# Optimization experiments

Hardware: AMD Instinct MI355X
Metric: run time of the kernel (lower is better)

The kernel has to match this reference:

```python
import jax, jax.numpy as jnp
import numpy as np

B, N1, N2, D, R = 4, 128, 128, 256, 4


def setup_inputs() -> dict:
    key = jax.random.key(0)
    ks = jax.random.split(key, 8)
    s = 0.02  # small init scale for weights
    return {
        "features1": jax.random.normal(ks[0], (B, N1, D), jnp.float32),
        "features2": jax.random.normal(ks[1], (B, N2, D), jnp.float32),
        # relation nets stacked over R: Linear(2D->D), Linear(D->D//2), Linear(D//2->1)
        "W1": jax.random.normal(ks[2], (R, 2 * D, D), jnp.float32) * s,
        "b1": jnp.zeros((R, D), jnp.float32),
        "W2": jax.random.normal(ks[3], (R, D, D // 2), jnp.float32) * s,
        "b2": jnp.zeros((R, D // 2), jnp.float32),
        "w3": jax.random.normal(ks[4], (R, D // 2), jnp.float32) * s,
        "b3": jnp.zeros((R,), jnp.float32),
        # aggregator: Linear(D*R -> 2D), Linear(2D -> D)
        "Wa1": jax.random.normal(ks[5], (D * R, 2 * D), jnp.float32) * s,
        "ba1": jnp.zeros((2 * D,), jnp.float32),
        "Wa2": jax.random.normal(ks[6], (2 * D, D), jnp.float32) * s,
        "ba2": jnp.zeros((D,), jnp.float32),
    }


def reference(features1, features2, W1, b1, W2, b2, w3, b3, Wa1, ba1, Wa2, ba2):
    b, n1, d = features1.shape
    n2 = features2.shape[1]
    r = W1.shape[0]
    # concat([f1_i, f2_j]) @ W1 == f1_i @ W1[:d] + f2_j @ W1[d:]
    W1a, W1b = W1[:, :d, :], W1[:, d:, :]
    h1 = jnp.einsum('bid,rde->brie', features1, W1a)          # [B,R,N1,D]
    h2 = jnp.einsum('bjd,rde->brje', features2, W1b)          # [B,R,N2,D]
    h = jax.nn.relu(h1[:, :, :, None, :] + h2[:, :, None, :, :]
                    + b1[None, :, None, None, :])             # [B,R,N1,N2,D]
    g = jax.nn.relu(jnp.einsum('brijd,rde->brije', h, W2)
                    + b2[None, :, None, None, :])             # [B,R,N1,N2,D//2]
    scores = jnp.einsum('brije,re->brij', g, w3) + b3[None, :, None, None]
    w = jax.nn.softmax(scores, axis=-1)                       # softmax over j (N2)
    rel = jnp.einsum('brij,bjd->brid', w, features2)          # [B,R,N1,D]
    # torch cat over relations along feature dim -> relation index outermost
    all_rel = rel.transpose(0, 2, 1, 3).reshape(b, n1, r * d)  # [B,N1,R*D]
    out = jax.nn.relu(all_rel @ Wa1 + ba1) @ Wa2 + ba2         # [B,N1,D]
    return out
```

## Files before the change

kernel.cpp:

```cpp
#include <hip/hip_runtime.h>


typedef _Float16 f16x8 __attribute__((ext_vector_type(8)));
typedef float f32x16 __attribute__((ext_vector_type(16)));

static __device__ __forceinline__ ushort f2h(float f) {
  _Float16 h = (_Float16)f;
  return __builtin_bit_cast(ushort, h);
}
static __device__ __forceinline__ uint pack2(float a, float b) {
  return (uint)f2h(a) | ((uint)f2h(b) << 16);
}
static __device__ __forceinline__ uint pk_add(uint a, uint b) {
  uint r;
  asm("v_pk_add_f16 %0, %1, %2" : "=v"(r) : "v"(a), "v"(b));
  return r;
}
static __device__ __forceinline__ uint pk_relu(uint a) {
  uint r;
  asm("v_pk_max_f16 %0, %1, %2" : "=v"(r) : "v"(a), "v"(0u));
  return r;
}

template<int KBLK>
static __device__ __forceinline__ void gemm32x64_body(
    const float* __restrict__ A, const float* __restrict__ W,
    float* __restrict__ Cout, int K, int N, int rt, int ct, int k0)
{
  int t = threadIdx.x;
  int tm2 = t >> 4;
  int tn4 = t & 15;
  int arow = t >> 3;
  int akq = (t & 7) * 4;
  int bk = t >> 4;
  int bn4 = (t & 15) * 4;
  __shared__ __align__(16) float As[32][33];
  __shared__ __align__(16) float Bs[32][64];

  const float* Ab = A + (size_t)(rt * 32 + arow) * K + k0;
  const float* Wb = W + (size_t)k0 * N + ct * 64 + bn4;

  float4 pa = *(const float4*)&Ab[akq];
  float4 pb0 = *(const float4*)&Wb[(size_t)bk * N];
  float4 pb1 = *(const float4*)&Wb[(size_t)(bk + 16) * N];

  float acc[2][4];
  #pragma unroll
  for (int i = 0; i < 2; ++i)
    #pragma unroll
    for (int j = 0; j < 4; ++j) acc[i][j] = 0.f;

  for (int kc = 0; kc < KBLK; kc += 32) {
    __syncthreads();
    As[akq + 0][arow] = pa.x;
    As[akq + 1][arow] = pa.y;
    As[akq + 2][arow] = pa.z;
    As[akq + 3][arow] = pa.w;
    *(float4*)&Bs[bk][bn4] = pb0;
    *(float4*)&Bs[bk + 16][bn4] = pb1;
    __syncthreads();
    if (kc + 32 < KBLK) {
      pa  = *(const float4*)&Ab[kc + 32 + akq];
      pb0 = *(const float4*)&Wb[(size_t)(kc + 32 + bk) * N];
      pb1 = *(const float4*)&Wb[(size_t)(kc + 32 + bk + 16) * N];
    }
    #pragma unroll
    for (int kk = 0; kk < 32; ++kk) {
      float2 a = *(const float2*)&As[kk][tm2 * 2];
      float4 w = *(const float4*)&Bs[kk][tn4 * 4];
      acc[0][0] = fmaf(a.x, w.x, acc[0][0]); acc[0][1] = fmaf(a.x, w.y, acc[0][1]);
      acc[0][2] = fmaf(a.x, w.z, acc[0][2]); acc[0][3] = fmaf(a.x, w.w, acc[0][3]);
      acc[1][0] = fmaf(a.y, w.x, acc[1][0]); acc[1][1] = fmaf(a.y, w.y, acc[1][1]);
      acc[1][2] = fmaf(a.y, w.z, acc[1][2]); acc[1][3] = fmaf(a.y, w.w, acc[1][3]);
    }
  }

  int col = ct * 64 + tn4 * 4;
  #pragma unroll
  for (int qm = 0; qm < 2; ++qm) {
    int row = rt * 32 + tm2 * 2 + qm;
    float4 ov = make_float4(acc[qm][0], acc[qm][1], acc[qm][2], acc[qm][3]);
    *(float4*)&Cout[(size_t)row * N + col] = ov;
  }
}

template<int KBLK>
__global__ __launch_bounds__(256) void gemm_part(
    const float* __restrict__ A, const float* __restrict__ W,
    float* __restrict__ part, int K, int N, int M)
{
  int kp = blockIdx.z;
  gemm32x64_body<KBLK>(A, W, part + (size_t)kp * M * N, K, N,
                       blockIdx.y, blockIdx.x, kp * KBLK);
}

__global__ __launch_bounds__(256) void gemm2_fused(
    const float* __restrict__ p1, const float* __restrict__ ba1,
    const float* __restrict__ W, float* __restrict__ part)
{
  const int K = 512, N = 256, KBLK = 128;
  int rt = blockIdx.y, ct = blockIdx.x, kp = blockIdx.z;
  int k0 = kp * KBLK;
  float* Cout = part + (size_t)kp * 512 * N;
  int t = threadIdx.x;
  int tm2 = t >> 4;
  int tn4 = t & 15;
  int arow = t >> 3;
  int akq = (t & 7) * 4;
  int bk = t >> 4;
  int bn4 = (t & 15) * 4;
  __shared__ __align__(16) float As[32][33];
  __shared__ __align__(16) float Bs[32][64];

  const float* Ap = p1 + (size_t)(rt * 32 + arow) * K;
  const float* Wb = W + (size_t)k0 * N + ct * 64 + bn4;

  auto loadA = [&](int k) -> float4 {
    float4 s  = *(const float4*)&Ap[k];
    float4 v1 = *(const float4*)&Ap[262144 + k];
    float4 v2 = *(const float4*)&Ap[524288 + k];
    float4 v3 = *(const float4*)&Ap[786432 + k];
    float4 bv = *(const float4*)&ba1[k];
    s.x = fmaxf(s.x + v1.x + v2.x + v3.x + bv.x, 0.f);
    s.y = fmaxf(s.y + v1.y + v2.y + v3.y + bv.y, 0.f);
    s.z = fmaxf(s.z + v1.z + v2.z + v3.z + bv.z, 0.f);
    s.w = fmaxf(s.w + v1.w + v2.w + v3.w + bv.w, 0.f);
    return s;
  };

  float4 pa = loadA(k0 + akq);
  float4 pb0 = *(const float4*)&Wb[(size_t)bk * N];
  float4 pb1 = *(const float4*)&Wb[(size_t)(bk + 16) * N];

  float acc[2][4];
  #pragma unroll
  for (int i = 0; i < 2; ++i)
    #pragma unroll
    for (int j = 0; j < 4; ++j) acc[i][j] = 0.f;

  for (int kc = 0; kc < KBLK; kc += 32) {
    __syncthreads();
    As[akq + 0][arow] = pa.x;
    As[akq + 1][arow] = pa.y;
    As[akq + 2][arow] = pa.z;
    As[akq + 3][arow] = pa.w;
    *(float4*)&Bs[bk][bn4] = pb0;
    *(float4*)&Bs[bk + 16][bn4] = pb1;
    __syncthreads();
    if (kc + 32 < KBLK) {
      pa  = loadA(k0 + kc + 32 + akq);
      pb0 = *(const float4*)&Wb[(size_t)(kc + 32 + bk) * N];
      pb1 = *(const float4*)&Wb[(size_t)(kc + 32 + bk + 16) * N];
    }
    #pragma unroll
    for (int kk = 0; kk < 32; ++kk) {
      float2 a = *(const float2*)&As[kk][tm2 * 2];
      float4 w = *(const float4*)&Bs[kk][tn4 * 4];
      acc[0][0] = fmaf(a.x, w.x, acc[0][0]); acc[0][1] = fmaf(a.x, w.y, acc[0][1]);
      acc[0][2] = fmaf(a.x, w.z, acc[0][2]); acc[0][3] = fmaf(a.x, w.w, acc[0][3]);
      acc[1][0] = fmaf(a.y, w.x, acc[1][0]); acc[1][1] = fmaf(a.y, w.y, acc[1][1]);
      acc[1][2] = fmaf(a.y, w.z, acc[1][2]); acc[1][3] = fmaf(a.y, w.w, acc[1][3]);
    }
  }

  int col = ct * 64 + tn4 * 4;
  #pragma unroll
  for (int qm = 0; qm < 2; ++qm) {
    int row = rt * 32 + tm2 * 2 + qm;
    float4 ov = make_float4(acc[qm][0], acc[qm][1], acc[qm][2], acc[qm][3]);
    *(float4*)&Cout[(size_t)row * N + col] = ov;
  }
}

template<int P>
__global__ __launch_bounds__(256) void reduce_bias_act(
    const float* __restrict__ part, const float* __restrict__ bias,
    float* __restrict__ C, int MN, int N, int act)
{
  int idx4 = (blockIdx.x * 256 + threadIdx.x) * 4;
  if (idx4 >= MN) return;
  float4 s = *(const float4*)&part[idx4];
  #pragma unroll
  for (int p = 1; p < P; ++p) {
    float4 v = *(const float4*)&part[(size_t)p * MN + idx4];
    s.x += v.x; s.y += v.y; s.z += v.z; s.w += v.w;
  }
  float4 bv = *(const float4*)&bias[idx4 & (N - 1)];
  s.x += bv.x; s.y += bv.y; s.z += bv.z; s.w += bv.w;
  if (act) {
    s.x = fmaxf(s.x, 0.f); s.y = fmaxf(s.y, 0.f);
    s.z = fmaxf(s.z, 0.f); s.w = fmaxf(s.w, 0.f);
  }
  *(float4*)&C[idx4] = s;
}

__global__ __launch_bounds__(256) void k_proj_w2(
    const float* __restrict__ f1, const float* __restrict__ f2,
    const float* __restrict__ W1, const float* __restrict__ b1,
    const float* __restrict__ W2, ushort* __restrict__ W2swz,
    ushort* __restrict__ f2swz,
    ushort* __restrict__ h1p, ushort* __restrict__ h2)
{
  int z = blockIdx.z;
  int t = threadIdx.x;
  __shared__ __align__(16) float As[32][33];
  __shared__ __align__(16) float Bs[32][64];

  if (z == 32) {
    int sub = blockIdx.y * 4 + blockIdx.x;
    int r = sub >> 2, ks0 = (sub & 3) * 4;
    int ct = t >> 6, l = t & 63;
    #pragma unroll
    for (int ko = 0; ko < 4; ++ko) {
      int ks = ks0 + ko;
      ushort us[8];
      #pragma unroll
      for (int j = 0; j < 8; ++j) {
        int d = ks * 16 + ((j >> 2) * 8) + ((l >> 5) * 4) + (j & 3);
        int e = ct * 32 + (l & 31);
        us[j] = f2h(W2[(r * 256 + d) * 128 + e]);
      }
      uint4 pk;
      pk.x = (uint)us[0] | ((uint)us[1] << 16);
      pk.y = (uint)us[2] | ((uint)us[3] << 16);
      pk.z = (uint)us[4] | ((uint)us[5] << 16);
      pk.w = (uint)us[6] | ((uint)us[7] << 16);
      *(uint4*)&W2swz[(((r * 16 + ks) * 4 + ct) * 64 + l) * 8] = pk;
    }
    return;
  }
  if (z == 33) {
    int sub = blockIdx.y * 4 + blockIdx.x;
    int w = t >> 6, l = t & 63;
    #pragma unroll
    for (int ko = 0; ko < 4; ++ko) {
      int u = sub * 16 + w * 4 + ko;
      int b = u >> 6, ks = (u >> 3) & 7, ctg = u & 7;
      ushort us[8];
      #pragma unroll
      for (int j = 0; j < 8; ++j) {
        int k = ks * 16 + ((l >> 5) * 4) + (j & 3) + ((j >> 2) * 8);
        int n = ctg * 32 + (l & 31);
        us[j] = f2h(f2[((size_t)b * 128 + k) * 256 + n]);
      }
      uint4 pk;
      pk.x = (uint)us[0] | ((uint)us[1] << 16);
      pk.y = (uint)us[2] | ((uint)us[3] << 16);
      pk.z = (uint)us[4] | ((uint)us[5] << 16);
      pk.w = (uint)us[6] | ((uint)us[7] << 16);
      *(uint4*)&f2swz[(((b * 8 + ks) * 8 + ctg) * 64 + l) * 8] = pk;
    }
    return;
  }

  int half = z >> 4, b = (z >> 2) & 3, r = z & 3;
  int rt = blockIdx.y, ct = blockIdx.x;
  int tm2 = t >> 4, tn4 = t & 15;
  int arow = t >> 3, akq = (t & 7) * 4;
  int bk = t >> 4, bn4 = (t & 15) * 4;

  const float* A = (half ? f2 : f1) + (size_t)b * 128 * 256;
  const float* W = W1 + (size_t)(r * 512 + half * 256) * 256;
  const float* Ab = A + (rt * 32 + arow) * 256;
  const float* Wb = W + ct * 64 + bn4;

  float4 pa = *(const float4*)&Ab[akq];
  float4 pb0 = *(const float4*)&Wb[bk * 256];
  float4 pb1 = *(const float4*)&Wb[(bk + 16) * 256];

  float acc[2][4];
  #pragma unroll
  for (int i = 0; i < 2; ++i)
    #pragma unroll
    for (int j = 0; j < 4; ++j) acc[i][j] = 0.f;

  for (int kc = 0; kc < 256; kc += 32) {
    __syncthreads();
    As[akq + 0][arow] = pa.x;
    As[akq + 1][arow] = pa.y;
    As[akq + 2][arow] = pa.z;
    As[akq + 3][arow] = pa.w;
    *(float4*)&Bs[bk][bn4] = pb0;
    *(float4*)&Bs[bk + 16][bn4] = pb1;
    __syncthreads();
    if (kc + 32 < 256) {
      pa  = *(const float4*)&Ab[kc + 32 + akq];
      pb0 = *(const float4*)&Wb[(kc + 32 + bk) * 256];
      pb1 = *(const float4*)&Wb[(kc + 32 + bk + 16) * 256];
    }
    #pragma unroll
    for (int kk = 0; kk < 32; ++kk) {
      float2 a = *(const float2*)&As[kk][tm2 * 2];
      float4 w = *(const float4*)&Bs[kk][tn4 * 4];
      acc[0][0] = fmaf(a.x, w.x, acc[0][0]); acc[0][1] = fmaf(a.x, w.y, acc[0][1]);
      acc[0][2] = fmaf(a.x, w.z, acc[0][2]); acc[0][3] = fmaf(a.x, w.w, acc[0][3]);
      acc[1][0] = fmaf(a.y, w.x, acc[1][0]); acc[1][1] = fmaf(a.y, w.y, acc[1][1]);
      acc[1][2] = fmaf(a.y, w.z, acc[1][2]); acc[1][3] = fmaf(a.y, w.w, acc[1][3]);
    }
  }

  int col = ct * 64 + tn4 * 4;
  float4 bv;
  if (half) { bv.x = bv.y = bv.z = bv.w = 0.f; }
  else      { bv = *(const float4*)&b1[r * 256 + col]; }
  uint* hu = (uint*)(half ? h2 : h1p);
  #pragma unroll
  for (int qm = 0; qm < 2; ++qm) {
    int row = rt * 32 + tm2 * 2 + qm;
    uint2 pv;
    pv.x = pack2(acc[qm][0] + bv.x, acc[qm][1] + bv.y);
    pv.y = pack2(acc[qm][2] + bv.z, acc[qm][3] + bv.w);
    *(uint2*)&hu[((size_t)((b * 4 + r) * 128 + row)) * 128 + (col >> 1)] = pv;
  }
}

__global__ __launch_bounds__(256, 4) void k_scores_mfma(
    const ushort* __restrict__ h1p, const ushort* __restrict__ h2,
    const ushort* __restrict__ W2swz, const float* __restrict__ b2,
    const float* __restrict__ w3, const float* __restrict__ b3,
    float* __restrict__ scores)
{
  int bid = blockIdx.x;
  int jt = bid & 7;
  int it = (bid >> 3) & 15;
  int r  = (bid >> 7) & 3;
  int b  = bid >> 9;
  int t = threadIdx.x, w = t >> 6, l = t & 63;
  __shared__ uint h1u[8][132];
  __shared__ uint h2u[16][132];
  __shared__ float xch[4][2][2][16];

  const uint* h1g = (const uint*)h1p + ((size_t)((b * 4 + r) * 128 + it * 8)) * 128;
  const uint* h2g = (const uint*)h2  + ((size_t)((b * 4 + r) * 128 + jt * 16)) * 128;
  {
    int row = t >> 5, c4 = (t & 31) * 4;
    *(uint4*)&h1u[row][c4] = *(const uint4*)&h1g[row * 128 + c4];
    *(uint4*)&h2u[row][c4] = *(const uint4*)&h2g[row * 128 + c4];
    *(uint4*)&h2u[row + 8][c4] = *(const uint4*)&h2g[(row + 8) * 128 + c4];
  }

  f32x16 acc[2][2];
  #pragma unroll
  for (int i = 0; i < 2; ++i)
    #pragma unroll
    for (int c = 0; c < 2; ++c)
      #pragma unroll
      for (int e = 0; e < 16; ++e) acc[i][c][e] = 0.f;

  int rtp = w & 1, ctp = w >> 1;
  int hi2 = (l >> 5) * 2;
  int m31 = l & 31;
  int jrow = m31 & 15;
  int irow0 = (rtp * 2 + 0) * 2 + (m31 >> 4);
  int irow1 = (rtp * 2 + 1) * 2 + (m31 >> 4);
  const ushort* bptr = W2swz + r * (16 * 4 * 64 * 8);

  __syncthreads();

  const uint* h1r0 = &h1u[irow0][0];
  const uint* h1r1 = &h1u[irow1][0];
  const uint* h2r  = &h2u[jrow][0];
  for (int ks = 0; ks < 16; ++ks) {
    int u0 = ks * 8 + hi2;
    uint2 ya  = *(const uint2*)&h2r[u0];
    uint2 yb  = *(const uint2*)&h2r[u0 + 4];
    uint2 xa0 = *(const uint2*)&h1r0[u0];
    uint2 xb0 = *(const uint2*)&h1r0[u0 + 4];
    uint2 xa1 = *(const uint2*)&h1r1[u0];
    uint2 xb1 = *(const uint2*)&h1r1[u0 + 4];
    uint4 pk0, pk1;
    pk0.x = pk_relu(pk_add(xa0.x, ya.x));
    pk0.y = pk_relu(pk_add(xa0.y, ya.y));
    pk0.z = pk_relu(pk_add(xb0.x, yb.x));
    pk0.w = pk_relu(pk_add(xb0.y, yb.y));
    pk1.x = pk_relu(pk_add(xa1.x, ya.x));
    pk1.y = pk_relu(pk_add(xa1.y, ya.y));
    pk1.z = pk_relu(pk_add(xb1.x, yb.x));
    pk1.w = pk_relu(pk_add(xb1.y, yb.y));
    f16x8 af0 = __builtin_bit_cast(f16x8, pk0);
    f16x8 af1 = __builtin_bit_cast(f16x8, pk1);
    uint4 braw0 = *(const uint4*)&bptr[((ks * 4 + ctp * 2 + 0) * 64 + l) * 8];
    uint4 braw1 = *(const uint4*)&bptr[((ks * 4 + ctp * 2 + 1) * 64 + l) * 8];
    f16x8 bf0 = __builtin_bit_cast(f16x8, braw0);
    f16x8 bf1 = __builtin_bit_cast(f16x8, braw1);
    acc[0][0] = __builtin_amdgcn_mfma_f32_32x32x16_f16(af0, bf0, acc[0][0], 0, 0, 0);
    acc[0][1] = __builtin_amdgcn_mfma_f32_32x32x16_f16(af0, bf1, acc[0][1], 0, 0, 0);
    acc[1][0] = __builtin_amdgcn_mfma_f32_32x32x16_f16(af1, bf0, acc[1][0], 0, 0, 0);
    acc[1][1] = __builtin_amdgcn_mfma_f32_32x32x16_f16(af1, bf1, acc[1][1], 0, 0, 0);
  }

  float sp[2][16];
  #pragma unroll
  for (int i = 0; i < 2; ++i)
    #pragma unroll
    for (int g = 0; g < 16; ++g) sp[i][g] = 0.f;
  #pragma unroll
  for (int ctl = 0; ctl < 2; ++ctl) {
    int e = (ctp * 2 + ctl) * 32 + m31;
    float w3v = w3[r * 128 + e];
    float b2v = b2[r * 128 + e];
    #pragma unroll
    for (int i = 0; i < 2; ++i)
      #pragma unroll
      for (int g = 0; g < 16; ++g)
        sp[i][g] = fmaf(w3v, fmaxf(acc[i][ctl][g] + b2v, 0.f), sp[i][g]);
  }
  #pragma unroll
  for (int off = 16; off >= 1; off >>= 1)
    #pragma unroll
    for (int i = 0; i < 2; ++i)
      #pragma unroll
      for (int g = 0; g < 16; ++g)
        sp[i][g] += __shfl_xor(sp[i][g], off, 64);
  int hi = l >> 5;
  if (m31 == 0) {
    #pragma unroll
    for (int i = 0; i < 2; ++i)
      #pragma unroll
      for (int g = 0; g < 16; ++g)
        xch[w][i][hi][g] = sp[i][g];
  }
  __syncthreads();
  if (w < 2 && m31 == 0) {
    float b3v = b3[r];
    float* sc_base = scores + (((b * 4 + r) * 128 + it * 8) * 128) + jt * 16;
    #pragma unroll
    for (int i = 0; i < 2; ++i)
      #pragma unroll
      for (int g = 0; g < 16; ++g) {
        float s = xch[w][i][hi][g] + xch[w + 2][i][hi][g] + b3v;
        int p = (w * 2 + i) * 32 + (g & 3) + 8 * (g >> 2) + hi * 4;
        sc_base[(p >> 4) * 128 + (p & 15)] = s;
      }
  }
}

__global__ __launch_bounds__(64, 1) void k_softrel_mfma(
    const float* __restrict__ scores, const ushort* __restrict__ f2swz,
    float* __restrict__ all_rel)
{
  int bid = blockIdx.x;
  int rowq = bid & 3;
  int nh = (bid >> 2) & 1;
  int r  = (bid >> 3) & 3;
  int b  = bid >> 5;
  int l = threadIdx.x;
  int row = rowq * 32 + (l & 31);
  const float* srow = scores + ((size_t)(b * 4 + r) * 128 + row) * 128;

  float p[128];
  #pragma unroll
  for (int q = 0; q < 32; ++q) {
    float4 v = *(const float4*)&srow[q * 4];
    p[q * 4 + 0] = v.x; p[q * 4 + 1] = v.y;
    p[q * 4 + 2] = v.z; p[q * 4 + 3] = v.w;
  }
  float m = p[0];
  #pragma unroll
  for (int j = 1; j < 128; ++j) m = fmaxf(m, p[j]);
  float sum = 0.f;
  #pragma unroll
  for (int j = 0; j < 128; ++j) { p[j] = __expf(p[j] - m); sum += p[j]; }
  float inv = 1.f / sum;
  uint preg[64];
  #pragma unroll
  for (int q = 0; q < 64; ++q)
    preg[q] = pack2(p[2 * q] * inv, p[2 * q + 1] * inv);

  f32x16 acc[4];
  #pragma unroll
  for (int c = 0; c < 4; ++c)
    #pragma unroll
    for (int e = 0; e < 16; ++e) acc[c][e] = 0.f;

  int hi2 = (l >> 5) * 2;
  const ushort* bbase = f2swz + (size_t)b * (8 * 8 * 64 * 8);
  #pragma unroll
  for (int ks = 0; ks < 8; ++ks) {
    int b2i = ks * 8 + hi2;
    uint4 pk = make_uint4(preg[b2i], preg[b2i + 1], preg[b2i + 4], preg[b2i + 5]);
    f16x8 af = __builtin_bit_cast(f16x8, pk);
    #pragma unroll
    for (int ct = 0; ct < 4; ++ct) {
      uint4 braw = *(const uint4*)&bbase[((ks * 8 + nh * 4 + ct) * 64 + l) * 8];
      f16x8 bfr = __builtin_bit_cast(f16x8, braw);
      acc[ct] = __builtin_amdgcn_mfma_f32_32x32x16_f16(af, bfr, acc[ct], 0, 0, 0);
    }
  }

  int dbase = r * 256 + nh * 128 + (l & 31);
  int half4 = (l >> 5) << 2;
  #pragma unroll
  for (int ct = 0; ct < 4; ++ct)
    #pragma unroll
    for (int g = 0; g < 16; ++g) {
      int i = rowq * 32 + (g & 3) + 8 * (g >> 2) + half4;
      all_rel[((size_t)(b * 128 + i)) * 1024 + dbase + ct * 32] = acc[ct][g];
    }
}

extern "C" void kernel_launch(void* const* d_in, const int* in_sizes, int n_in,
                              void* d_out, int out_size, void* d_ws, size_t ws_size,
                              hipStream_t stream) {
  const float* f1  = (const float*)d_in[0];
  const float* f2  = (const float*)d_in[1];
  const float* W1  = (const float*)d_in[2];
  const float* b1  = (const float*)d_in[3];
  const float* W2  = (const float*)d_in[4];
  const float* b2  = (const float*)d_in[5];
  const float* w3  = (const float*)d_in[6];
  const float* b3  = (const float*)d_in[7];
  const float* Wa1 = (const float*)d_in[8];
  const float* ba1 = (const float*)d_in[9];
  const float* Wa2 = (const float*)d_in[10];
  const float* ba2 = (const float*)d_in[11];
  float* out = (float*)d_out;
  float* ws = (float*)d_ws;

  ushort* h1p    = (ushort*)ws;
  ushort* h2     = (ushort*)(ws + 262144);
  float* scores  = ws + 524288;
  float* all_rel = ws + 1048576;
  ushort* W2swz  = (ushort*)(ws + 1835008);
  ushort* f2swz  = (ushort*)(ws + 1900544);
  float* p1      = ws + 2097152;
  float* p2      = ws + 3145728;

  hipLaunchKernelGGL(k_proj_w2, dim3(4, 4, 34), dim3(256), 0, stream,
                     f1, f2, W1, b1, W2, W2swz, f2swz, h1p, h2);
  hipLaunchKernelGGL(k_scores_mfma, dim3(2048), dim3(256), 0, stream,
                     h1p, h2, W2swz, b2, w3, b3, scores);
  hipLaunchKernelGGL(k_softrel_mfma, dim3(128), dim3(64), 0, stream,
                     scores, f2swz, all_rel);
  hipLaunchKernelGGL((gemm_part<256>), dim3(8, 16, 4), dim3(256), 0, stream,
                     all_rel, Wa1, p1, 1024, 512, 512);
  hipLaunchKernelGGL(gemm2_fused, dim3(4, 16, 4), dim3(256), 0, stream,
                     p1, ba1, Wa2, p2);
  hipLaunchKernelGGL((reduce_bias_act<4>), dim3(128), dim3(256), 0, stream,
                     p2, ba2, out, 512 * 256, 256, 0);
}
```

Baseline: 76.50 us.

## Fuse aggregator MLP into one fp16 MFMA kernel with pre-swizzled weights

Replaces the three-launch fp32 split-K aggregator (two SIMT GEMMs plus a reduce) with one kernel that runs both aggregator layers on fp16 MFMA. The hidden activations stay in LDS. Wa1 and Wa2 are converted to fp16 and swizzled by extra blocks of the first kernel, and all_rel is now written as fp16. This removes two launches, the partial-sum traffic, and scalar FMA GEMMs. In exchange the MLP runs on only 16 blocks, which limits parallelism, and fp16 rounding is added to the aggregator path.

```diff
diff --git a/kernel.cpp b/kernel.cpp
--- a/kernel.cpp
+++ b/kernel.cpp
@@ -22,183 +22,13 @@
   return r;
 }
 
-template<int KBLK>
-static __device__ __forceinline__ void gemm32x64_body(
-    const float* __restrict__ A, const float* __restrict__ W,
-    float* __restrict__ Cout, int K, int N, int rt, int ct, int k0)
-{
-  int t = threadIdx.x;
-  int tm2 = t >> 4;
-  int tn4 = t & 15;
-  int arow = t >> 3;
-  int akq = (t & 7) * 4;
-  int bk = t >> 4;
-  int bn4 = (t & 15) * 4;
-  __shared__ __align__(16) float As[32][33];
-  __shared__ __align__(16) float Bs[32][64];
-
-  const float* Ab = A + (size_t)(rt * 32 + arow) * K + k0;
-  const float* Wb = W + (size_t)k0 * N + ct * 64 + bn4;
-
-  float4 pa = *(const float4*)&Ab[akq];
-  float4 pb0 = *(const float4*)&Wb[(size_t)bk * N];
-  float4 pb1 = *(const float4*)&Wb[(size_t)(bk + 16) * N];
-
-  float acc[2][4];
-  #pragma unroll
-  for (int i = 0; i < 2; ++i)
-    #pragma unroll
-    for (int j = 0; j < 4; ++j) acc[i][j] = 0.f;
-
-  for (int kc = 0; kc < KBLK; kc += 32) {
-    __syncthreads();
-    As[akq + 0][arow] = pa.x;
-    As[akq + 1][arow] = pa.y;
-    As[akq + 2][arow] = pa.z;
-    As[akq + 3][arow] = pa.w;
-    *(float4*)&Bs[bk][bn4] = pb0;
-    *(float4*)&Bs[bk + 16][bn4] = pb1;
-    __syncthreads();
-    if (kc + 32 < KBLK) {
-      pa  = *(const float4*)&Ab[kc + 32 + akq];
-      pb0 = *(const float4*)&Wb[(size_t)(kc + 32 + bk) * N];
-      pb1 = *(const float4*)&Wb[(size_t)(kc + 32 + bk + 16) * N];
-    }
-    #pragma unroll
-    for (int kk = 0; kk < 32; ++kk) {
-      float2 a = *(const float2*)&As[kk][tm2 * 2];
-      float4 w = *(const float4*)&Bs[kk][tn4 * 4];
-      acc[0][0] = fmaf(a.x, w.x, acc[0][0]); acc[0][1] = fmaf(a.x, w.y, acc[0][1]);
-      acc[0][2] = fmaf(a.x, w.z, acc[0][2]); acc[0][3] = fmaf(a.x, w.w, acc[0][3]);
-      acc[1][0] = fmaf(a.y, w.x, acc[1][0]); acc[1][1] = fmaf(a.y, w.y, acc[1][1]);
-      acc[1][2] = fmaf(a.y, w.z, acc[1][2]); acc[1][3] = fmaf(a.y, w.w, acc[1][3]);
-    }
-  }
-
-  int col = ct * 64 + tn4 * 4;
-  #pragma unroll
-  for (int qm = 0; qm < 2; ++qm) {
-    int row = rt * 32 + tm2 * 2 + qm;
-    float4 ov = make_float4(acc[qm][0], acc[qm][1], acc[qm][2], acc[qm][3]);
-    *(float4*)&Cout[(size_t)row * N + col] = ov;
-  }
-}
-
-template<int KBLK>
-__global__ __launch_bounds__(256) void gemm_part(
-    const float* __restrict__ A, const float* __restrict__ W,
-    float* __restrict__ part, int K, int N, int M)
-{
-  int kp = blockIdx.z;
-  gemm32x64_body<KBLK>(A, W, part + (size_t)kp * M * N, K, N,
-                       blockIdx.y, blockIdx.x, kp * KBLK);
-}
-
-__global__ __launch_bounds__(256) void gemm2_fused(
-    const float* __restrict__ p1, const float* __restrict__ ba1,
-    const float* __restrict__ W, float* __restrict__ part)
-{
-  const int K = 512, N = 256, KBLK = 128;
-  int rt = blockIdx.y, ct = blockIdx.x, kp = blockIdx.z;
-  int k0 = kp * KBLK;
-  float* Cout = part + (size_t)kp * 512 * N;
-  int t = threadIdx.x;
-  int tm2 = t >> 4;
-  int tn4 = t & 15;
-  int arow = t >> 3;
-  int akq = (t & 7) * 4;
-  int bk = t >> 4;
-  int bn4 = (t & 15) * 4;
-  __shared__ __align__(16) float As[32][33];
-  __shared__ __align__(16) float Bs[32][64];
-
-  const float* Ap = p1 + (size_t)(rt * 32 + arow) * K;
-  const float* Wb = W + (size_t)k0 * N + ct * 64 + bn4;
-
-  auto loadA = [&](int k) -> float4 {
-    float4 s  = *(const float4*)&Ap[k];
-    float4 v1 = *(const float4*)&Ap[262144 + k];
-    float4 v2 = *(const float4*)&Ap[524288 + k];
-    float4 v3 = *(const float4*)&Ap[786432 + k];
-    float4 bv = *(const float4*)&ba1[k];
-    s.x = fmaxf(s.x + v1.x + v2.x + v3.x + bv.x, 0.f);
-    s.y = fmaxf(s.y + v1.y + v2.y + v3.y + bv.y, 0.f);
-    s.z = fmaxf(s.z + v1.z + v2.z + v3.z + bv.z, 0.f);
-    s.w = fmaxf(s.w + v1.w + v2.w + v3.w + bv.w, 0.f);
-    return s;
-  };
-
-  float4 pa = loadA(k0 + akq);
-  float4 pb0 = *(const float4*)&Wb[(size_t)bk * N];
-  float4 pb1 = *(const float4*)&Wb[(size_t)(bk + 16) * N];
-
-  float acc[2][4];
-  #pragma unroll
-  for (int i = 0; i < 2; ++i)
-    #pragma unroll
-    for (int j = 0; j < 4; ++j) acc[i][j] = 0.f;
-
-  for (int kc = 0; kc < KBLK; kc += 32) {
-    __syncthreads();
-    As[akq + 0][arow] = pa.x;
-    As[akq + 1][arow] = pa.y;
-    As[akq + 2][arow] = pa.z;
-    As[akq + 3][arow] = pa.w;
-    *(float4*)&Bs[bk][bn4] = pb0;
-    *(float4*)&Bs[bk + 16][bn4] = pb1;
-    __syncthreads();
-    if (kc + 32 < KBLK) {
-      pa  = loadA(k0 + kc + 32 + akq);
-      pb0 = *(const float4*)&Wb[(size_t)(kc + 32 + bk) * N];
-      pb1 = *(const float4*)&Wb[(size_t)(kc + 32 + bk + 16) * N];
-    }
-    #pragma unroll
-    for (int kk = 0; kk < 32; ++kk) {
-      float2 a = *(const float2*)&As[kk][tm2 * 2];
-      float4 w = *(const float4*)&Bs[kk][tn4 * 4];
-      acc[0][0] = fmaf(a.x, w.x, acc[0][0]); acc[0][1] = fmaf(a.x, w.y, acc[0][1]);
-      acc[0][2] = fmaf(a.x, w.z, acc[0][2]); acc[0][3] = fmaf(a.x, w.w, acc[0][3]);
-      acc[1][0] = fmaf(a.y, w.x, acc[1][0]); acc[1][1] = fmaf(a.y, w.y, acc[1][1]);
-      acc[1][2] = fmaf(a.y, w.z, acc[1][2]); acc[1][3] = fmaf(a.y, w.w, acc[1][3]);
-    }
-  }
-
-  int col = ct * 64 + tn4 * 4;
-  #pragma unroll
-  for (int qm = 0; qm < 2; ++qm) {
-    int row = rt * 32 + tm2 * 2 + qm;
-    float4 ov = make_float4(acc[qm][0], acc[qm][1], acc[qm][2], acc[qm][3]);
-    *(float4*)&Cout[(size_t)row * N + col] = ov;
-  }
-}
-
-template<int P>
-__global__ __launch_bounds__(256) void reduce_bias_act(
-    const float* __restrict__ part, const float* __restrict__ bias,
-    float* __restrict__ C, int MN, int N, int act)
-{
-  int idx4 = (blockIdx.x * 256 + threadIdx.x) * 4;
-  if (idx4 >= MN) return;
-  float4 s = *(const float4*)&part[idx4];
-  #pragma unroll
-  for (int p = 1; p < P; ++p) {
-    float4 v = *(const float4*)&part[(size_t)p * MN + idx4];
-    s.x += v.x; s.y += v.y; s.z += v.z; s.w += v.w;
-  }
-  float4 bv = *(const float4*)&bias[idx4 & (N - 1)];
-  s.x += bv.x; s.y += bv.y; s.z += bv.z; s.w += bv.w;
-  if (act) {
-    s.x = fmaxf(s.x, 0.f); s.y = fmaxf(s.y, 0.f);
-    s.z = fmaxf(s.z, 0.f); s.w = fmaxf(s.w, 0.f);
-  }
-  *(float4*)&C[idx4] = s;
-}
-
 __global__ __launch_bounds__(256) void k_proj_w2(
     const float* __restrict__ f1, const float* __restrict__ f2,
     const float* __restrict__ W1, const float* __restrict__ b1,
-    const float* __restrict__ W2, ushort* __restrict__ W2swz,
-    ushort* __restrict__ f2swz,
+    const float* __restrict__ W2, const float* __restrict__ Wa1,
+    const float* __restrict__ Wa2,
+    ushort* __restrict__ W2swz, ushort* __restrict__ f2swz,
+    ushort* __restrict__ Wa1swz, ushort* __restrict__ Wa2swz,
     ushort* __restrict__ h1p, ushort* __restrict__ h2)
 {
   int z = blockIdx.z;
@@ -213,18 +43,16 @@
     #pragma unroll
     for (int ko = 0; ko < 4; ++ko) {
       int ks = ks0 + ko;
-      ushort us[8];
-      #pragma unroll
-      for (int j = 0; j < 8; ++j) {
-        int d = ks * 16 + ((j >> 2) * 8) + ((l >> 5) * 4) + (j & 3);
+      uint4 pk;
+      uint* pw = (uint*)&pk;
+      #pragma unroll
+      for (int jp = 0; jp < 4; ++jp) {
+        int j0 = jp * 2;
+        int d0 = ks * 16 + ((j0 >> 2) * 8) + ((l >> 5) * 4) + (j0 & 3);
+        int d1 = ks * 16 + (((j0 + 1) >> 2) * 8) + ((l >> 5) * 4) + ((j0 + 1) & 3);
         int e = ct * 32 + (l & 31);
-        us[j] = f2h(W2[(r * 256 + d) * 128 + e]);
+        pw[jp] = pack2(W2[(r * 256 + d0) * 128 + e], W2[(r * 256 + d1) * 128 + e]);
       }
-      uint4 pk;
-      pk.x = (uint)us[0] | ((uint)us[1] << 16);
-      pk.y = (uint)us[2] | ((uint)us[3] << 16);
-      pk.z = (uint)us[4] | ((uint)us[5] << 16);
-      pk.w = (uint)us[6] | ((uint)us[7] << 16);
       *(uint4*)&W2swz[(((r * 16 + ks) * 4 + ct) * 64 + l) * 8] = pk;
     }
     return;
@@ -249,6 +77,50 @@
       pk.z = (uint)us[4] | ((uint)us[5] << 16);
       pk.w = (uint)us[6] | ((uint)us[7] << 16);
       *(uint4*)&f2swz[(((b * 8 + ks) * 8 + ctg) * 64 + l) * 8] = pk;
+    }
+    return;
+  }
+  if (z == 34) {
+    int sub = blockIdx.y * 4 + blockIdx.x;
+    #pragma unroll
+    for (int ko = 0; ko < 16; ++ko) {
+      int id = sub * 4096 + ko * 256 + t;
+      int ks = id >> 10, ct = (id >> 6) & 15, l = id & 63;
+      ushort us[8];
+      #pragma unroll
+      for (int j = 0; j < 8; ++j) {
+        int d = ks * 16 + ((l >> 5) * 4) + (j & 3) + ((j >> 2) * 8);
+        int e = ct * 32 + (l & 31);
+        us[j] = f2h(Wa1[(size_t)d * 512 + e]);
+      }
+      uint4 pk;
+      pk.x = (uint)us[0] | ((uint)us[1] << 16);
+      pk.y = (uint)us[2] | ((uint)us[3] << 16);
+      pk.z = (uint)us[4] | ((uint)us[5] << 16);
+      pk.w = (uint)us[6] | ((uint)us[7] << 16);
+      *(uint4*)&Wa1swz[(size_t)id * 8] = pk;
+    }
+    return;
+  }
+  if (z == 35) {
+    int sub = blockIdx.y * 4 + blockIdx.x;
+    #pragma unroll
+    for (int ko = 0; ko < 4; ++ko) {
+      int id = sub * 1024 + ko * 256 + t;
+      int ks = id >> 9, ct = (id >> 6) & 7, l = id & 63;
+      ushort us[8];
+      #pragma unroll
+      for (int j = 0; j < 8; ++j) {
+        int d = ks * 16 + ((l >> 5) * 4) + (j & 3) + ((j >> 2) * 8);
+        int e = ct * 32 + (l & 31);
+        us[j] = f2h(Wa2[(size_t)d * 256 + e]);
+      }
+      uint4 pk;
+      pk.x = (uint)us[0] | ((uint)us[1] << 16);
+      pk.y = (uint)us[2] | ((uint)us[3] << 16);
+      pk.z = (uint)us[4] | ((uint)us[5] << 16);
+      pk.w = (uint)us[6] | ((uint)us[7] << 16);
+      *(uint4*)&Wa2swz[(size_t)id * 8] = pk;
     }
     return;
   }
@@ -437,7 +309,7 @@
 
 __global__ __launch_bounds__(64, 1) void k_softrel_mfma(
     const float* __restrict__ scores, const ushort* __restrict__ f2swz,
-    float* __restrict__ all_rel)
+    ushort* __restrict__ all_rel_h)
 {
   int bid = blockIdx.x;
   int rowq = bid & 3;
@@ -488,15 +360,91 @@
     }
   }
 
-  int dbase = r * 256 + nh * 128 + (l & 31);
+  ushort* dst = all_rel_h + (size_t)(b * 128) * 1024;
+  int ebase = r * 256 + nh * 128 + (l & 31);
   int half4 = (l >> 5) << 2;
   #pragma unroll
   for (int ct = 0; ct < 4; ++ct)
     #pragma unroll
     for (int g = 0; g < 16; ++g) {
       int i = rowq * 32 + (g & 3) + 8 * (g >> 2) + half4;
-      all_rel[((size_t)(b * 128 + i)) * 1024 + dbase + ct * 32] = acc[ct][g];
-    }
+      dst[(size_t)i * 1024 + ebase + ct * 32] = f2h(acc[ct][g]);
+    }
+}
+
+__global__ __launch_bounds__(512) void k_mlp(
+    const ushort* __restrict__ all_rel_h, const ushort* __restrict__ Wa1swz,
+    const float* __restrict__ ba1, const ushort* __restrict__ Wa2swz,
+    const float* __restrict__ ba2, float* __restrict__ out)
+{
+  int b0 = blockIdx.x;
+  int t = threadIdx.x, w = t >> 6, l = t & 63;
+  __shared__ uint Ah[32][514];
+  __shared__ uint Hh[32][258];
+
+  const uint* Ag = (const uint*)all_rel_h + (size_t)b0 * 32 * 512;
+  #pragma unroll
+  for (int it = 0; it < 8; ++it) {
+    int idx = it * 512 + t;
+    int row = idx >> 7, c2 = (idx & 127) * 4;
+    uint2 v0 = *(const uint2*)&Ag[row * 512 + c2];
+    uint2 v1 = *(const uint2*)&Ag[row * 512 + c2 + 2];
+    *(uint2*)&Ah[row][c2] = v0;
+    *(uint2*)&Ah[row][c2 + 2] = v1;
+  }
+  __syncthreads();
+
+  int m31 = l & 31, hi = l >> 5, hi2 = hi * 2;
+
+  f32x16 acc0, acc1;
+  #pragma unroll
+  for (int e = 0; e < 16; ++e) { acc0[e] = 0.f; acc1[e] = 0.f; }
+  for (int ks = 0; ks < 64; ++ks) {
+    int u0 = ks * 8 + hi2;
+    uint2 xa = *(const uint2*)&Ah[m31][u0];
+    uint2 xb = *(const uint2*)&Ah[m31][u0 + 4];
+    uint4 a4 = make_uint4(xa.x, xa.y, xb.x, xb.y);
+    f16x8 af = __builtin_bit_cast(f16x8, a4);
+    uint4 braw0 = *(const uint4*)&Wa1swz[(size_t)(((ks * 16 + w * 2 + 0) * 64 + l)) * 8];
+    uint4 braw1 = *(const uint4*)&Wa1swz[(size_t)(((ks * 16 + w * 2 + 1) * 64 + l)) * 8];
+    f16x8 bf0 = __builtin_bit_cast(f16x8, braw0);
+    f16x8 bf1 = __builtin_bit_cast(f16x8, braw1);
+    acc0 = __builtin_amdgcn_mfma_f32_32x32x16_f16(af, bf0, acc0, 0, 0, 0);
+    acc1 = __builtin_amdgcn_mfma_f32_32x32x16_f16(af, bf1, acc1, 0, 0, 0);
+  }
+  ushort* Hs = (ushort*)Hh;
+  #pragma unroll
+  for (int ctl = 0; ctl < 2; ++ctl) {
+    int e = (w * 2 + ctl) * 32 + m31;
+    float bv = ba1[e];
+    #pragma unroll
+    for (int g = 0; g < 16; ++g) {
+      int row = (g & 3) + 8 * (g >> 2) + 4 * hi;
+      float v = fmaxf((ctl ? acc1[g] : acc0[g]) + bv, 0.f);
+      Hs[row * 516 + e] = f2h(v);
+    }
+  }
+  __syncthreads();
+
+  f32x16 acc2;
+  #pragma unroll
+  for (int e = 0; e < 16; ++e) acc2[e] = 0.f;
+  for (int ks = 0; ks < 32; ++ks) {
+    int u0 = ks * 8 + hi2;
+    uint2 xa = *(const uint2*)&Hh[m31][u0];
+    uint2 xb = *(const uint2*)&Hh[m31][u0 + 4];
+    uint4 a4 = make_uint4(xa.x, xa.y, xb.x, xb.y);
+    f16x8 af = __builtin_bit_cast(f16x8, a4);
+    uint4 braw = *(const uint4*)&Wa2swz[(size_t)(((ks * 8 + w) * 64 + l)) * 8];
+    f16x8 bfr = __builtin_bit_cast(f16x8, braw);
+    acc2 = __builtin_amdgcn_mfma_f32_32x32x16_f16(af, bfr, acc2, 0, 0, 0);
+  }
+  float bv2 = ba2[w * 32 + m31];
+  #pragma unroll
+  for (int g = 0; g < 16; ++g) {
+    int row = (g & 3) + 8 * (g >> 2) + 4 * hi;
+    out[(size_t)(b0 * 32 + row) * 256 + w * 32 + m31] = acc2[g] + bv2;
+  }
 }
 
 extern "C" void kernel_launch(void* const* d_in, const int* in_sizes, int n_in,
@@ -517,25 +465,22 @@
   float* out = (float*)d_out;
   float* ws = (float*)d_ws;
 
-  ushort* h1p    = (ushort*)ws;
-  ushort* h2     = (ushort*)(ws + 262144);
-  float* scores  = ws + 524288;
-  float* all_rel = ws + 1048576;
-  ushort* W2swz  = (ushort*)(ws + 1835008);
-  ushort* f2swz  = (ushort*)(ws + 1900544);
-  float* p1      = ws + 2097152;
-  float* p2      = ws + 3145728;
-
-  hipLaunchKernelGGL(k_proj_w2, dim3(4, 4, 34), dim3(256), 0, stream,
-                     f1, f2, W1, b1, W2, W2swz, f2swz, h1p, h2);
+  ushort* h1p      = (ushort*)ws;
+  ushort* h2       = (ushort*)(ws + 262144);
+  float*  scores   = ws + 524288;
+  ushort* all_relh = (ushort*)(ws + 786432);
+  ushort* W2swz    = (ushort*)(ws + 1048576);
+  ushort* f2swz    = (ushort*)(ws + 1114112);
+  ushort* Wa1swz   = (ushort*)(ws + 1179648);
+  ushort* Wa2swz   = (ushort*)(ws + 1441792);
+
+  hipLaunchKernelGGL(k_proj_w2, dim3(4, 4, 36), dim3(256), 0, stream,
+                     f1, f2, W1, b1, W2, Wa1, Wa2,
+                     W2swz, f2swz, Wa1swz, Wa2swz, h1p, h2);
   hipLaunchKernelGGL(k_scores_mfma, dim3(2048), dim3(256), 0, stream,
                      h1p, h2, W2swz, b2, w3, b3, scores);
   hipLaunchKernelGGL(k_softrel_mfma, dim3(128), dim3(64), 0, stream,
-                     scores, f2swz, all_rel);
-  hipLaunchKernelGGL((gemm_part<256>), dim3(8, 16, 4), dim3(256), 0, stream,
-                     all_rel, Wa1, p1, 1024, 512, 512);
-  hipLaunchKernelGGL(gemm2_fused, dim3(4, 16, 4), dim3(256), 0, stream,
-                     p1, ba1, Wa2, p2);
-  hipLaunchKernelGGL((reduce_bias_act<4>), dim3(128), dim3(256), 0, stream,
-                     p2, ba2, out, 512 * 256, 256, 0);
-}
+                     scores, f2swz, all_relh);
+  hipLaunchKernelGGL(k_mlp, dim3(16), dim3(512), 0, stream,
+                     all_relh, Wa1swz, ba1, Wa2swz, ba2, out);
+}
```

New measurement: 79.44 us. 1.04x slower.
